# Kernel optimization log

Measured on AMD Instinct MI355X. Metric: run time of the kernel, lower is better.

The kernel has to match this reference:

```python
import jax, jax.numpy as jnp
import numpy as np

STAGE_NUM = 3
BN_EPS = 1e-5


def _l2norm(x, axis):
    return x / (1e-6 + jnp.linalg.norm(x, axis=axis, keepdims=True))


def setup_inputs() -> dict:
    key = jax.random.key(0)
    b, c, k = 16, 256, 64
    sizes = [(80, 80), (40, 40), (20, 20), (10, 10)]
    ks = jax.random.split(key, 12)
    inp = {}
    for i, (h, w) in enumerate(sizes):
        inp[f"x{i}"] = jax.random.normal(ks[i], (b, c, h, w), dtype=jnp.float32)
    # 1x1 conv weights, kaiming-style init as in the module (n = out_channels)
    inp["w1"] = jax.random.normal(ks[8], (c, c), dtype=jnp.float32) * np.sqrt(2.0 / c)
    inp["b1"] = jnp.zeros((c,), dtype=jnp.float32)
    inp["w2"] = jax.random.normal(ks[9], (c, c), dtype=jnp.float32) * np.sqrt(2.0 / c)
    inp["bn_gamma"] = jnp.ones((c,), dtype=jnp.float32)
    inp["bn_beta"] = jnp.zeros((c,), dtype=jnp.float32)
    inp["bn_mean"] = jnp.zeros((c,), dtype=jnp.float32)
    inp["bn_var"] = jnp.ones((c,), dtype=jnp.float32)
    mu = jax.random.normal(ks[10], (1, c, k), dtype=jnp.float32) * np.sqrt(2.0 / k)
    inp["mu"] = _l2norm(mu, axis=1)
    return inp


def reference(x0, x1, x2, x3, w1, b1, w2, bn_gamma, bn_beta, bn_mean, bn_var, mu):
    xs = [x0, x1, x2, x3]
    b, c = x0.shape[0], x0.shape[1]
    idn = xs
    # conv1: 1x1 conv with bias == channel matmul
    xs = [jnp.einsum('oc,bchw->bohw', w1, x) + b1[None, :, None, None] for x in xs]
    sizes = [x.shape for x in xs]
    x_total = jnp.concatenate([x.reshape(b, c, -1) for x in xs], axis=-1)  # [b,c,N]
    k = mu.shape[-1]
    mu_b = jnp.broadcast_to(mu, (b, c, k))
    # EM iterations run under torch.no_grad() in the original -> stop_gradient
    xt = jax.lax.stop_gradient(x_total)
    z = None
    for _ in range(STAGE_NUM):
        z = jax.nn.softmax(jnp.einsum('bcn,bck->bnk', xt, mu_b), axis=2)  # [b,N,k]
        z_ = z / (1e-6 + z.sum(axis=1, keepdims=True))
        mu_b = _l2norm(jnp.einsum('bcn,bnk->bck', xt, z_), axis=1)
    # reconstruction: mu @ z^T, relu
    x_rec = jax.nn.relu(jnp.einsum('bck,bnk->bcn', mu_b, z))  # [b,c,N]
    outs = []
    cur = 0
    inv_std = (bn_gamma / jnp.sqrt(bn_var + BN_EPS))[None, :, None, None]
    shift = (bn_beta - bn_mean * bn_gamma / jnp.sqrt(bn_var + BN_EPS))[None, :, None, None]
    for i, s in enumerate(sizes):
        n = s[2] * s[3]
        term = x_rec[:, :, cur:cur + n].reshape(s)
        cur += n
        y = jnp.einsum('oc,bchw->bohw', w2, term)  # conv2 (no bias)
        y = y * inv_std + shift                    # eval-mode BatchNorm2d
        outs.append(jax.nn.relu(y + idn[i]))
    return (*outs, mu_b)
```

## Files before the change

### kernel.cpp

```cpp
#include <hip/hip_runtime.h>
#include <math.h>

#define NTOT 8500

__device__ __forceinline__ size_t in_index(int gn, int bc, int* which) {
  if (gn < 6400) { *which = 0; return (size_t)bc * 6400 + gn; }
  if (gn < 8000) { *which = 1; return (size_t)bc * 1600 + (gn - 6400); }
  if (gn < 8400) { *which = 2; return (size_t)bc * 400  + (gn - 8000); }
  *which = 3;     return (size_t)bc * 100  + (gn - 8400);
}

__global__ __launch_bounds__(256)
void concat_kernel(const float* __restrict__ x0, const float* __restrict__ x1,
                   const float* __restrict__ x2, const float* __restrict__ x3,
                   float* __restrict__ xcat)
{
  const int bc = blockIdx.y;
  const int gn = (blockIdx.x * 256 + threadIdx.x) * 4;
  if (gn >= NTOT) return;
  int w_; size_t idx = in_index(gn, bc, &w_);
  const float* src = (w_ == 0) ? x0 : (w_ == 1) ? x1 : (w_ == 2) ? x2 : x3;
  *(float4*)(xcat + (size_t)bc * NTOT + gn) = *(const float4*)(src + idx);
}

__global__ __launch_bounds__(256)
void conv2_kernel(const float* __restrict__ W,
                  const float* __restrict__ x0, const float* __restrict__ x1,
                  const float* __restrict__ x2, const float* __restrict__ x3,
                  const float* __restrict__ xrec,
                  const float* __restrict__ bn_g, const float* __restrict__ bn_b,
                  const float* __restrict__ bn_m, const float* __restrict__ bn_v,
                  float* __restrict__ out)
{
  __shared__ float As[32][68];
  __shared__ float Bs[32][132];
  const int t  = threadIdx.x;
  const int n0 = blockIdx.x * 128;
  const int m0 = blockIdx.y * 64;
  const int b  = blockIdx.z;
  const int tm = t & 15, tn = t >> 4;

  float acc[4][8];
#pragma unroll
  for (int i = 0; i < 4; ++i)
#pragma unroll
    for (int j = 0; j < 8; ++j) acc[i][j] = 0.f;

  for (int k0 = 0; k0 < 256; k0 += 32) {
#pragma unroll
    for (int it = 0; it < 2; ++it) {
      const int o_l = (t >> 3) + 32 * it;
      const int kk4 = (t & 7) * 4;
      float4 v = *(const float4*)(W + (size_t)(m0 + o_l) * 256 + k0 + kk4);
      As[kk4 + 0][o_l] = v.x; As[kk4 + 1][o_l] = v.y;
      As[kk4 + 2][o_l] = v.z; As[kk4 + 3][o_l] = v.w;
    }
#pragma unroll
    for (int it = 0; it < 4; ++it) {
      const int kk  = (t >> 5) + 8 * it;
      const int nn4 = (t & 31) * 4;
      const int gn  = n0 + nn4;
      float4 v = make_float4(0.f, 0.f, 0.f, 0.f);
      if (gn < NTOT)
        v = *(const float4*)(xrec + (size_t)(b * 256 + k0 + kk) * NTOT + gn);
      *(float4*)&Bs[kk][nn4] = v;
    }
    __syncthreads();
#pragma unroll
    for (int kk = 0; kk < 32; ++kk) {
      float4 a = *(const float4*)&As[kk][tm * 4];
      float4 p = *(const float4*)&Bs[kk][tn * 8];
      float4 q = *(const float4*)&Bs[kk][tn * 8 + 4];
      float av[4] = {a.x, a.y, a.z, a.w};
      float bv[8] = {p.x, p.y, p.z, p.w, q.x, q.y, q.z, q.w};
#pragma unroll
      for (int i = 0; i < 4; ++i)
#pragma unroll
        for (int j = 0; j < 8; ++j)
          acc[i][j] = fmaf(av[i], bv[j], acc[i][j]);
    }
    __syncthreads();
  }

#pragma unroll
  for (int i = 0; i < 4; ++i) {
    const int o = m0 + tm * 4 + i;
    float g   = bn_g[o];
    float isf = g / sqrtf(bn_v[o] + 1e-5f);
    float shf = bn_b[o] - bn_m[o] * isf;
#pragma unroll
    for (int jj = 0; jj < 8; jj += 4) {
      const int gn = n0 + tn * 8 + jj;
      if (gn >= NTOT) continue;
      float4 r = make_float4(acc[i][jj + 0], acc[i][jj + 1],
                             acc[i][jj + 2], acc[i][jj + 3]);
      int w_; size_t idx = in_index(gn, b * 256 + o, &w_);
      const float* src = (w_ == 0) ? x0 : (w_ == 1) ? x1 : (w_ == 2) ? x2 : x3;
      float4 rv = *(const float4*)(src + idx);
      size_t ob = (w_ == 0) ? 0ull : (w_ == 1) ? 26214400ull
                : (w_ == 2) ? 32768000ull : 34406400ull;
      r.x = fmaxf(fmaf(r.x, isf, shf) + rv.x, 0.f);
      r.y = fmaxf(fmaf(r.y, isf, shf) + rv.y, 0.f);
      r.z = fmaxf(fmaf(r.z, isf, shf) + rv.z, 0.f);
      r.w = fmaxf(fmaf(r.w, isf, shf) + rv.w, 0.f);
      *(float4*)(out + ob + idx) = r;
    }
  }
}

__global__ __launch_bounds__(256)
void transpose_kernel(const float* __restrict__ w1, float* __restrict__ w1t)
{
  __shared__ float tile[32][33];
  const int bx = blockIdx.x, by = blockIdx.y;
  const int tx = threadIdx.x & 31, ty = threadIdx.x >> 5;
#pragma unroll
  for (int j = 0; j < 32; j += 8)
    tile[ty + j][tx] = w1[(size_t)(by * 32 + ty + j) * 256 + bx * 32 + tx];
  __syncthreads();
#pragma unroll
  for (int j = 0; j < 32; j += 8)
    w1t[(size_t)(bx * 32 + ty + j) * 256 + by * 32 + tx] = tile[tx][ty + j];
}

__global__ __launch_bounds__(256)
void t0_kernel(const float* __restrict__ w1, const float* __restrict__ b1,
               const float* __restrict__ mu0, float* __restrict__ t0,
               float* __restrict__ s0)
{
  const int k = blockIdx.x, c = threadIdx.x;
  __shared__ float M[256];
  __shared__ float red[256];
  M[c] = mu0[(size_t)c * 64 + k];
  __syncthreads();
  float acc = 0.f;
#pragma unroll 8
  for (int cp = 0; cp < 256; ++cp)
    acc = fmaf(w1[(size_t)cp * 256 + c], M[cp], acc);
  t0[(size_t)c * 64 + k] = acc;
  red[c] = b1[c] * M[c];
  __syncthreads();
  for (int off = 128; off > 0; off >>= 1) {
    if (c < off) red[c] += red[c + off];
    __syncthreads();
  }
  if (c == 0) s0[k] = red[0];
}

__global__ __launch_bounds__(256)
void z_kernel(const float* __restrict__ xcat,
              const float* __restrict__ t, const float* __restrict__ s,
              int per_batch, float* __restrict__ zbuf)
{
  __shared__ float xs[32][136];
  __shared__ float mus[32][68];
  const int tid = threadIdx.x;
  const int n0 = blockIdx.x * 128;
  const int b  = blockIdx.y;
  const float* tb = t + (per_batch ? (size_t)b * 256 * 64 : 0);
  const float* sb = s + (per_batch ? (size_t)b * 64 : 0);
  const int tk = tid & 15, tn = tid >> 4;
  const float4 sv = *(const float4*)(sb + tk * 4);

  float acc[8][4];
#pragma unroll
  for (int r = 0; r < 8; ++r)
#pragma unroll
    for (int j = 0; j < 4; ++j) acc[r][j] = 0.f;

  for (int c0 = 0; c0 < 256; c0 += 32) {
#pragma unroll
    for (int it = 0; it < 4; ++it) {
      const int cc  = (tid >> 5) + 8 * it;
      const int nn4 = (tid & 31) * 4;
      const int gn  = n0 + nn4;
      float4 v = (gn < NTOT)
          ? *(const float4*)(xcat + (size_t)(b * 256 + c0 + cc) * NTOT + gn)
          : make_float4(0.f, 0.f, 0.f, 0.f);
      *(float4*)&xs[cc][nn4] = v;
    }
#pragma unroll
    for (int it = 0; it < 2; ++it) {
      const int cc  = (tid >> 4) + 16 * it;
      const int kk4 = (tid & 15) * 4;
      float4 v = *(const float4*)(tb + (size_t)(c0 + cc) * 64 + kk4);
      *(float4*)&mus[cc][kk4] = v;
    }
    __syncthreads();
#pragma unroll
    for (int cc = 0; cc < 32; ++cc) {
      float4 m4 = *(const float4*)&mus[cc][tk * 4];
      float4 xa = *(const float4*)&xs[cc][tn * 8];
      float4 xb = *(const float4*)&xs[cc][tn * 8 + 4];
      float xv[8] = {xa.x, xa.y, xa.z, xa.w, xb.x, xb.y, xb.z, xb.w};
      float mv[4] = {m4.x, m4.y, m4.z, m4.w};
#pragma unroll
      for (int r = 0; r < 8; ++r)
#pragma unroll
        for (int j = 0; j < 4; ++j)
          acc[r][j] = fmaf(xv[r], mv[j], acc[r][j]);
    }
    __syncthreads();
  }

#pragma unroll
  for (int r = 0; r < 8; ++r) {
    acc[r][0] += sv.x; acc[r][1] += sv.y; acc[r][2] += sv.z; acc[r][3] += sv.w;
    float mx = fmaxf(fmaxf(acc[r][0], acc[r][1]), fmaxf(acc[r][2], acc[r][3]));
#pragma unroll
    for (int off = 8; off >= 1; off >>= 1) mx = fmaxf(mx, __shfl_xor(mx, off));
    float e0 = __expf(acc[r][0] - mx), e1 = __expf(acc[r][1] - mx);
    float e2 = __expf(acc[r][2] - mx), e3 = __expf(acc[r][3] - mx);
    float ssum = e0 + e1 + e2 + e3;
#pragma unroll
    for (int off = 8; off >= 1; off >>= 1) ssum += __shfl_xor(ssum, off);
    const float inv = 1.0f / ssum;
    const int gn = n0 + tn * 8 + r;
    if (gn < NTOT) {
      float4 w = make_float4(e0 * inv, e1 * inv, e2 * inv, e3 * inv);
      *(float4*)(zbuf + ((size_t)b * NTOT + gn) * 64 + tk * 4) = w;
    }
  }
}

__global__ __launch_bounds__(256)
void mu_part_kernel(const float* __restrict__ xcat,
                    const float* __restrict__ z, float* __restrict__ part,
                    float* __restrict__ csum)
{
  __shared__ float As[32][132];
  __shared__ float Bs[32][68];
  const int t  = threadIdx.x;
  const int ch = blockIdx.x;
  const int c0 = blockIdx.y * 128;
  const int b  = blockIdx.z;
  const int nb = ch * 512;
  const int tk = t & 15, tc = t >> 4;
  const bool do_cs = (blockIdx.y == 0);

  float acc[8][4];
#pragma unroll
  for (int i = 0; i < 8; ++i)
#pragma unroll
    for (int j = 0; j < 4; ++j) acc[i][j] = 0.f;
  float cs[4] = {0.f, 0.f, 0.f, 0.f};

  for (int kb = 0; kb < 512; kb += 32) {
#pragma unroll
    for (int it = 0; it < 4; ++it) {
      const int c_l = (t >> 3) + 32 * it;
      const int nn4 = (t & 7) * 4;
      const int gn  = nb + kb + nn4;
      float4 v = (gn < NTOT)
          ? *(const float4*)(xcat + (size_t)(b * 256 + c0 + c_l) * NTOT + gn)
          : make_float4(0.f, 0.f, 0.f, 0.f);
      As[nn4 + 0][c_l] = v.x; As[nn4 + 1][c_l] = v.y;
      As[nn4 + 2][c_l] = v.z; As[nn4 + 3][c_l] = v.w;
    }
#pragma unroll
    for (int it = 0; it < 2; ++it) {
      const int nn  = (t >> 4) + 16 * it;
      const int kk4 = (t & 15) * 4;
      const int gn  = nb + kb + nn;
      float4 v = (gn < NTOT)
          ? *(const float4*)(z + ((size_t)b * NTOT + gn) * 64 + kk4)
          : make_float4(0.f, 0.f, 0.f, 0.f);
      *(float4*)&Bs[nn][kk4] = v;
    }
    __syncthreads();
    if (do_cs && tc == 0) {
#pragma unroll
      for (int nn = 0; nn < 32; ++nn) {
#pragma unroll
        for (int j = 0; j < 4; ++j) cs[j] += Bs[nn][tk * 4 + j];
      }
    }
#pragma unroll
    for (int nn = 0; nn < 32; ++nn) {
      float4 a0 = *(const float4*)&As[nn][tc * 8];
      float4 a1 = *(const float4*)&As[nn][tc * 8 + 4];
      float4 bz = *(const float4*)&Bs[nn][tk * 4];
      float av[8] = {a0.x, a0.y, a0.z, a0.w, a1.x, a1.y, a1.z, a1.w};
      float bv[4] = {bz.x, bz.y, bz.z, bz.w};
#pragma unroll
      for (int i = 0; i < 8; ++i)
#pragma unroll
        for (int j = 0; j < 4; ++j)
          acc[i][j] = fmaf(av[i], bv[j], acc[i][j]);
    }
    __syncthreads();
  }

#pragma unroll
  for (int j = 0; j < 4; ++j) {
    const int k = tk * 4 + j;
    float4 v0 = make_float4(acc[0][j], acc[1][j], acc[2][j], acc[3][j]);
    float4 v1 = make_float4(acc[4][j], acc[5][j], acc[6][j], acc[7][j]);
    size_t base = (((size_t)b * 17 + ch) * 64 + k) * 256 + c0 + tc * 8;
    *(float4*)(part + base)     = v0;
    *(float4*)(part + base + 4) = v1;
  }
  if (do_cs && tc == 0) {
#pragma unroll
    for (int j = 0; j < 4; ++j)
      csum[((size_t)b * 17 + ch) * 64 + tk * 4 + j] = cs[j];
  }
}

__global__ __launch_bounds__(256)
void mu_solve_kernel(const float* __restrict__ part, const float* __restrict__ csum,
                     const float* __restrict__ w1t, const float* __restrict__ w1,
                     const float* __restrict__ b1,
                     float* __restrict__ muws, float* __restrict__ tbuf,
                     float* __restrict__ sbuf, float* __restrict__ mu_out)
{
  const int k = blockIdx.x, b = blockIdx.y, c = threadIdx.x;
  __shared__ float Y[256];
  __shared__ float M[256];
  __shared__ float red[256];

  float y = 0.f;
  for (int ch = 0; ch < 17; ++ch)
    y += part[(((size_t)b * 17 + ch) * 64 + k) * 256 + c];
  Y[c] = y;
  float csv = 0.f;
  for (int ch = 0; ch < 17; ++ch)
    csv += csum[((size_t)b * 17 + ch) * 64 + k];
  __syncthreads();

  float acc = 0.f;
#pragma unroll 8
  for (int cp = 0; cp < 256; ++cp)
    acc = fmaf(w1t[(size_t)cp * 256 + c], Y[cp], acc);
  acc = fmaf(b1[c], csv, acc);

  red[c] = acc * acc;
  __syncthreads();
  for (int off = 128; off > 0; off >>= 1) {
    if (c < off) red[c] += red[c + off];
    __syncthreads();
  }
  const float val = acc / (1e-6f + sqrtf(red[0]));
  M[c] = val;
  muws[((size_t)b * 256 + c) * 64 + k] = val;
  if (mu_out) mu_out[((size_t)b * 256 + c) * 64 + k] = val;
  __syncthreads();

  float acc2 = 0.f;
#pragma unroll 8
  for (int cp = 0; cp < 256; ++cp)
    acc2 = fmaf(w1[(size_t)cp * 256 + c], M[cp], acc2);
  tbuf[((size_t)b * 256 + c) * 64 + k] = acc2;

  red[c] = b1[c] * val;
  __syncthreads();
  for (int off = 128; off > 0; off >>= 1) {
    if (c < off) red[c] += red[c + off];
    __syncthreads();
  }
  if (c == 0) sbuf[(size_t)b * 64 + k] = red[0];
}

__global__ __launch_bounds__(256)
void rec_kernel(const float* __restrict__ mu, const float* __restrict__ z,
                float* __restrict__ xrec)
{
  __shared__ float As[16][68];
  __shared__ float Bs[16][132];
  const int t  = threadIdx.x;
  const int n0 = blockIdx.x * 128;
  const int c0 = blockIdx.y * 64;
  const int b  = blockIdx.z;
  const int tm = t & 15, tn = t >> 4;

  float acc[4][8];
#pragma unroll
  for (int i = 0; i < 4; ++i)
#pragma unroll
    for (int j = 0; j < 8; ++j) acc[i][j] = 0.f;

  for (int k0 = 0; k0 < 64; k0 += 16) {
    {
      const int c_l = t >> 2;
      const int kk4 = (t & 3) * 4;
      float4 v = *(const float4*)(mu + ((size_t)(b * 256 + c0 + c_l)) * 64 + k0 + kk4);
      As[kk4 + 0][c_l] = v.x; As[kk4 + 1][c_l] = v.y;
      As[kk4 + 2][c_l] = v.z; As[kk4 + 3][c_l] = v.w;
    }
#pragma unroll
    for (int it = 0; it < 2; ++it) {
      const int nn  = (t >> 2) + 64 * it;
      const int kk4 = (t & 3) * 4;
      const int gn  = n0 + nn;
      float4 v = (gn < NTOT)
          ? *(const float4*)(z + ((size_t)b * NTOT + gn) * 64 + k0 + kk4)
          : make_float4(0.f, 0.f, 0.f, 0.f);
      Bs[kk4 + 0][nn] = v.x; Bs[kk4 + 1][nn] = v.y;
      Bs[kk4 + 2][nn] = v.z; Bs[kk4 + 3][nn] = v.w;
    }
    __syncthreads();
#pragma unroll
    for (int kk = 0; kk < 16; ++kk) {
      float4 a = *(const float4*)&As[kk][tm * 4];
      float4 p = *(const float4*)&Bs[kk][tn * 8];
      float4 q = *(const float4*)&Bs[kk][tn * 8 + 4];
      float av[4] = {a.x, a.y, a.z, a.w};
      float bv[8] = {p.x, p.y, p.z, p.w, q.x, q.y, q.z, q.w};
#pragma unroll
      for (int i = 0; i < 4; ++i)
#pragma unroll
        for (int j = 0; j < 8; ++j)
          acc[i][j] = fmaf(av[i], bv[j], acc[i][j]);
    }
    __syncthreads();
  }

#pragma unroll
  for (int i = 0; i < 4; ++i) {
    const int cc = c0 + tm * 4 + i;
#pragma unroll
    for (int jj = 0; jj < 8; jj += 4) {
      const int gn = n0 + tn * 8 + jj;
      if (gn >= NTOT) continue;
      float4 r = make_float4(fmaxf(acc[i][jj + 0], 0.f), fmaxf(acc[i][jj + 1], 0.f),
                             fmaxf(acc[i][jj + 2], 0.f), fmaxf(acc[i][jj + 3], 0.f));
      *(float4*)(xrec + (size_t)(b * 256 + cc) * NTOT + gn) = r;
    }
  }
}

extern "C" void kernel_launch(void* const* d_in, const int* in_sizes, int n_in,
                              void* d_out, int out_size, void* d_ws, size_t ws_size,
                              hipStream_t stream)
{
  const float* x0   = (const float*)d_in[0];
  const float* x1   = (const float*)d_in[1];
  const float* x2   = (const float*)d_in[2];
  const float* x3   = (const float*)d_in[3];
  const float* w1   = (const float*)d_in[4];
  const float* b1   = (const float*)d_in[5];
  const float* w2   = (const float*)d_in[6];
  const float* bn_g = (const float*)d_in[7];
  const float* bn_b = (const float*)d_in[8];
  const float* bn_m = (const float*)d_in[9];
  const float* bn_v = (const float*)d_in[10];
  const float* mu0  = (const float*)d_in[11];
  float* out = (float*)d_out;

  float* xcat = (float*)d_ws;
  float* z    = xcat + 34816000ull;
  float* part = z    + 8704000ull;
  float* muws = part + 4456448ull;
  float* tbuf = muws + 262144ull;
  float* sbuf = tbuf + 262144ull;
  float* t0b  = sbuf + 1024ull;
  float* s0b  = t0b  + 16384ull;
  float* csum = s0b  + 64ull;
  float* w1t  = csum + 17408ull;

  concat_kernel<<<dim3(9, 4096), 256, 0, stream>>>(x0, x1, x2, x3, xcat);
  transpose_kernel<<<dim3(8, 8), 256, 0, stream>>>(w1, w1t);
  t0_kernel<<<64, 256, 0, stream>>>(w1, b1, mu0, t0b, s0b);

  for (int s = 0; s < 3; ++s) {
    z_kernel<<<dim3(67, 16), 256, 0, stream>>>(
        xcat, s == 0 ? t0b : tbuf, s == 0 ? s0b : sbuf, s == 0 ? 0 : 1, z);
    mu_part_kernel<<<dim3(17, 2, 16), 256, 0, stream>>>(
        xcat, z, part, csum);
    mu_solve_kernel<<<dim3(64, 16), 256, 0, stream>>>(
        part, csum, w1t, w1, b1, muws, tbuf, sbuf,
        (s == 2) ? (out + 34816000ull) : nullptr);
  }
  rec_kernel<<<dim3(67, 4, 16), 256, 0, stream>>>(muws, z, xcat);
  conv2_kernel<<<dim3(67, 4, 16), 256, 0, stream>>>(
      w2, x0, x1, x2, x3, xcat, bn_g, bn_b, bn_m, bn_v, out);
}
```

Before: 1.137 ms.

## Run conv2 on bf16 MFMA with split hi/lo precision and transposed xrec layout

Replaces the FP32 SIMT conv2 GEMM with a bf16 MFMA kernel. It emulates near-fp32 accuracy by splitting both operands into high and low bf16 parts and issuing three MFMAs per tile. rec_kernel now writes the reconstruction as hi/lo bf16 in an [b, n, c] layout so the MFMA B operand loads contiguously along K, and a small kernel pre-splits w2. The aim is to cut the conv2 FP32 FMA cost; in exchange the epilogue stores become scalar instead of float4, and rec_kernel does transposed strided stores.

```diff
diff --git a/kernel.cpp b/kernel.cpp
--- a/kernel.cpp
+++ b/kernel.cpp
@@ -2,6 +2,20 @@
 #include <math.h>
 
 #define NTOT 8500
+
+typedef unsigned short u16;
+typedef __attribute__((ext_vector_type(8))) short    bf16x8;
+typedef __attribute__((ext_vector_type(8))) unsigned short u16x8;
+typedef __attribute__((ext_vector_type(4))) float    f32x4;
+
+__device__ __forceinline__ u16 f2bf(float x) {
+  unsigned u = __float_as_uint(x);
+  u += 0x7FFFu + ((u >> 16) & 1u);
+  return (u16)(u >> 16);
+}
+__device__ __forceinline__ float bf2f(u16 h) {
+  return __uint_as_float(((unsigned)h) << 16);
+}
 
 __device__ __forceinline__ size_t in_index(int gn, int bc, int* which) {
   if (gn < 6400) { *which = 0; return (size_t)bc * 6400 + gn; }
@@ -24,86 +38,90 @@
 }
 
 __global__ __launch_bounds__(256)
-void conv2_kernel(const float* __restrict__ W,
-                  const float* __restrict__ x0, const float* __restrict__ x1,
-                  const float* __restrict__ x2, const float* __restrict__ x3,
-                  const float* __restrict__ xrec,
-                  const float* __restrict__ bn_g, const float* __restrict__ bn_b,
-                  const float* __restrict__ bn_m, const float* __restrict__ bn_v,
-                  float* __restrict__ out)
-{
-  __shared__ float As[32][68];
-  __shared__ float Bs[32][132];
+void w2cvt_kernel(const float* __restrict__ w2, u16* __restrict__ h,
+                  u16* __restrict__ l)
+{
+  const int i = blockIdx.x * 256 + threadIdx.x;
+  const float v = w2[i];
+  const u16 hh = f2bf(v);
+  h[i] = hh;
+  l[i] = f2bf(v - bf2f(hh));
+}
+
+__global__ __launch_bounds__(256)
+void conv2_mfma_kernel(const u16* __restrict__ w2h, const u16* __restrict__ w2l,
+                       const u16* __restrict__ xrh, const u16* __restrict__ xrl,
+                       const float* __restrict__ x0, const float* __restrict__ x1,
+                       const float* __restrict__ x2, const float* __restrict__ x3,
+                       const float* __restrict__ bn_g, const float* __restrict__ bn_b,
+                       const float* __restrict__ bn_m, const float* __restrict__ bn_v,
+                       float* __restrict__ out)
+{
+  __shared__ __align__(16) u16 Wh[64][40],  Wl[64][40];
+  __shared__ __align__(16) u16 Bh[128][40], Bl[128][40];
   const int t  = threadIdx.x;
   const int n0 = blockIdx.x * 128;
   const int m0 = blockIdx.y * 64;
   const int b  = blockIdx.z;
-  const int tm = t & 15, tn = t >> 4;
-
-  float acc[4][8];
-#pragma unroll
-  for (int i = 0; i < 4; ++i)
-#pragma unroll
-    for (int j = 0; j < 8; ++j) acc[i][j] = 0.f;
+  const int w  = t >> 6, lane = t & 63;
+  const int lr = lane & 15, lg = lane >> 4;
+
+  f32x4 acc[8];
+#pragma unroll
+  for (int nt = 0; nt < 8; ++nt) acc[nt] = (f32x4){0.f, 0.f, 0.f, 0.f};
 
   for (int k0 = 0; k0 < 256; k0 += 32) {
-#pragma unroll
-    for (int it = 0; it < 2; ++it) {
-      const int o_l = (t >> 3) + 32 * it;
-      const int kk4 = (t & 7) * 4;
-      float4 v = *(const float4*)(W + (size_t)(m0 + o_l) * 256 + k0 + kk4);
-      As[kk4 + 0][o_l] = v.x; As[kk4 + 1][o_l] = v.y;
-      As[kk4 + 2][o_l] = v.z; As[kk4 + 3][o_l] = v.w;
-    }
-#pragma unroll
-    for (int it = 0; it < 4; ++it) {
-      const int kk  = (t >> 5) + 8 * it;
-      const int nn4 = (t & 31) * 4;
-      const int gn  = n0 + nn4;
-      float4 v = make_float4(0.f, 0.f, 0.f, 0.f);
-      if (gn < NTOT)
-        v = *(const float4*)(xrec + (size_t)(b * 256 + k0 + kk) * NTOT + gn);
-      *(float4*)&Bs[kk][nn4] = v;
-    }
-    __syncthreads();
-#pragma unroll
-    for (int kk = 0; kk < 32; ++kk) {
-      float4 a = *(const float4*)&As[kk][tm * 4];
-      float4 p = *(const float4*)&Bs[kk][tn * 8];
-      float4 q = *(const float4*)&Bs[kk][tn * 8 + 4];
-      float av[4] = {a.x, a.y, a.z, a.w};
-      float bv[8] = {p.x, p.y, p.z, p.w, q.x, q.y, q.z, q.w};
-#pragma unroll
-      for (int i = 0; i < 4; ++i)
-#pragma unroll
-        for (int j = 0; j < 8; ++j)
-          acc[i][j] = fmaf(av[i], bv[j], acc[i][j]);
-    }
-    __syncthreads();
-  }
-
-#pragma unroll
-  for (int i = 0; i < 4; ++i) {
-    const int o = m0 + tm * 4 + i;
-    float g   = bn_g[o];
-    float isf = g / sqrtf(bn_v[o] + 1e-5f);
-    float shf = bn_b[o] - bn_m[o] * isf;
-#pragma unroll
-    for (int jj = 0; jj < 8; jj += 4) {
-      const int gn = n0 + tn * 8 + jj;
+    {
+      const int row = t >> 2, cb = (t & 3) * 8;
+      const size_t g = (size_t)(m0 + row) * 256 + k0 + cb;
+      *(u16x8*)&Wh[row][cb] = *(const u16x8*)(w2h + g);
+      *(u16x8*)&Wl[row][cb] = *(const u16x8*)(w2l + g);
+    }
+    {
+      const int row = t >> 1, cb = (t & 1) * 16;
+      const int gn  = n0 + row;
+      if (gn < NTOT) {
+        const size_t g = ((size_t)b * NTOT + gn) * 256 + k0 + cb;
+        *(u16x8*)&Bh[row][cb]     = *(const u16x8*)(xrh + g);
+        *(u16x8*)&Bh[row][cb + 8] = *(const u16x8*)(xrh + g + 8);
+        *(u16x8*)&Bl[row][cb]     = *(const u16x8*)(xrl + g);
+        *(u16x8*)&Bl[row][cb + 8] = *(const u16x8*)(xrl + g + 8);
+      } else {
+        const u16x8 zz = {0, 0, 0, 0, 0, 0, 0, 0};
+        *(u16x8*)&Bh[row][cb] = zz; *(u16x8*)&Bh[row][cb + 8] = zz;
+        *(u16x8*)&Bl[row][cb] = zz; *(u16x8*)&Bl[row][cb + 8] = zz;
+      }
+    }
+    __syncthreads();
+
+    const bf16x8 ah = *(const bf16x8*)&Wh[w * 16 + lr][lg * 8];
+    const bf16x8 al = *(const bf16x8*)&Wl[w * 16 + lr][lg * 8];
+#pragma unroll
+    for (int nt = 0; nt < 8; ++nt) {
+      const bf16x8 bh = *(const bf16x8*)&Bh[nt * 16 + lr][lg * 8];
+      const bf16x8 bl = *(const bf16x8*)&Bl[nt * 16 + lr][lg * 8];
+      acc[nt] = __builtin_amdgcn_mfma_f32_16x16x32_bf16(ah, bh, acc[nt], 0, 0, 0);
+      acc[nt] = __builtin_amdgcn_mfma_f32_16x16x32_bf16(ah, bl, acc[nt], 0, 0, 0);
+      acc[nt] = __builtin_amdgcn_mfma_f32_16x16x32_bf16(al, bh, acc[nt], 0, 0, 0);
+    }
+    __syncthreads();
+  }
+
+#pragma unroll
+  for (int r = 0; r < 4; ++r) {
+    const int o = m0 + w * 16 + lg * 4 + r;
+    const float g   = bn_g[o];
+    const float isf = g / sqrtf(bn_v[o] + 1e-5f);
+    const float shf = bn_b[o] - bn_m[o] * isf;
+#pragma unroll
+    for (int nt = 0; nt < 8; ++nt) {
+      const int gn = n0 + nt * 16 + lr;
       if (gn >= NTOT) continue;
-      float4 r = make_float4(acc[i][jj + 0], acc[i][jj + 1],
-                             acc[i][jj + 2], acc[i][jj + 3]);
       int w_; size_t idx = in_index(gn, b * 256 + o, &w_);
       const float* src = (w_ == 0) ? x0 : (w_ == 1) ? x1 : (w_ == 2) ? x2 : x3;
-      float4 rv = *(const float4*)(src + idx);
-      size_t ob = (w_ == 0) ? 0ull : (w_ == 1) ? 26214400ull
-                : (w_ == 2) ? 32768000ull : 34406400ull;
-      r.x = fmaxf(fmaf(r.x, isf, shf) + rv.x, 0.f);
-      r.y = fmaxf(fmaf(r.y, isf, shf) + rv.y, 0.f);
-      r.z = fmaxf(fmaf(r.z, isf, shf) + rv.z, 0.f);
-      r.w = fmaxf(fmaf(r.w, isf, shf) + rv.w, 0.f);
-      *(float4*)(out + ob + idx) = r;
+      const size_t ob = (w_ == 0) ? 0ull : (w_ == 1) ? 26214400ull
+                      : (w_ == 2) ? 32768000ull : 34406400ull;
+      out[ob + idx] = fmaxf(fmaf(acc[nt][r], isf, shf) + src[idx], 0.f);
     }
   }
 }
@@ -363,7 +381,7 @@
 
 __global__ __launch_bounds__(256)
 void rec_kernel(const float* __restrict__ mu, const float* __restrict__ z,
-                float* __restrict__ xrec)
+                u16* __restrict__ xrh, u16* __restrict__ xrl)
 {
   __shared__ float As[16][68];
   __shared__ float Bs[16][132];
@@ -416,16 +434,21 @@
   }
 
 #pragma unroll
-  for (int i = 0; i < 4; ++i) {
-    const int cc = c0 + tm * 4 + i;
-#pragma unroll
-    for (int jj = 0; jj < 8; jj += 4) {
-      const int gn = n0 + tn * 8 + jj;
-      if (gn >= NTOT) continue;
-      float4 r = make_float4(fmaxf(acc[i][jj + 0], 0.f), fmaxf(acc[i][jj + 1], 0.f),
-                             fmaxf(acc[i][jj + 2], 0.f), fmaxf(acc[i][jj + 3], 0.f));
-      *(float4*)(xrec + (size_t)(b * 256 + cc) * NTOT + gn) = r;
-    }
+  for (int j = 0; j < 8; ++j) {
+    const int gn = n0 + tn * 8 + j;
+    if (gn >= NTOT) continue;
+    const float v0 = fmaxf(acc[0][j], 0.f);
+    const float v1 = fmaxf(acc[1][j], 0.f);
+    const float v2 = fmaxf(acc[2][j], 0.f);
+    const float v3 = fmaxf(acc[3][j], 0.f);
+    ushort4 h, l;
+    h.x = f2bf(v0); l.x = f2bf(v0 - bf2f(h.x));
+    h.y = f2bf(v1); l.y = f2bf(v1 - bf2f(h.y));
+    h.z = f2bf(v2); l.z = f2bf(v2 - bf2f(h.z));
+    h.w = f2bf(v3); l.w = f2bf(v3 - bf2f(h.w));
+    const size_t base = ((size_t)b * NTOT + gn) * 256 + c0 + tm * 4;
+    *(ushort4*)(xrh + base) = h;
+    *(ushort4*)(xrl + base) = l;
   }
 }
 
@@ -457,10 +480,15 @@
   float* s0b  = t0b  + 16384ull;
   float* csum = s0b  + 64ull;
   float* w1t  = csum + 17408ull;
+  u16* xrh = (u16*)xcat;
+  u16* xrl = xrh + 34816000ull;
+  u16* w2h = (u16*)(w1t + 65536ull);
+  u16* w2l = w2h + 65536ull;
 
   concat_kernel<<<dim3(9, 4096), 256, 0, stream>>>(x0, x1, x2, x3, xcat);
   transpose_kernel<<<dim3(8, 8), 256, 0, stream>>>(w1, w1t);
   t0_kernel<<<64, 256, 0, stream>>>(w1, b1, mu0, t0b, s0b);
+  w2cvt_kernel<<<256, 256, 0, stream>>>(w2, w2h, w2l);
 
   for (int s = 0; s < 3; ++s) {
     z_kernel<<<dim3(67, 16), 256, 0, stream>>>(
@@ -471,7 +499,7 @@
         part, csum, w1t, w1, b1, muws, tbuf, sbuf,
         (s == 2) ? (out + 34816000ull) : nullptr);
   }
-  rec_kernel<<<dim3(67, 4, 16), 256, 0, stream>>>(muws, z, xcat);
-  conv2_kernel<<<dim3(67, 4, 16), 256, 0, stream>>>(
-      w2, x0, x1, x2, x3, xcat, bn_g, bn_b, bn_m, bn_v, out);
-}
+  rec_kernel<<<dim3(67, 4, 16), 256, 0, stream>>>(muws, z, xrh, xrl);
+  conv2_mfma_kernel<<<dim3(67, 4, 16), 256, 0, stream>>>(
+      w2h, w2l, xrh, xrl, x0, x1, x2, x3, bn_g, bn_b, bn_m, bn_v, out);
+}
```

Result: no change. 1.149 ms (+1.1%).
